# Performance work log

Measured on AMD Instinct MI355X. Metric: run time of the kernel, lower is better.

The kernel has to match this reference:

```python
import jax, jax.numpy as jnp
import numpy as np

B, L, H, D = 4096, 256, 32, 2
LOG_PROB_FACTOR = 0.5

def setup_inputs() -> dict:
    key = jax.random.key(0)
    k0, k1, k2, k3 = jax.random.split(key, 4)
    x = jax.random.randint(k0, (B, L), 0, D)  # spin configs in {0,1}
    Wi = jax.random.normal(k1, (D, 4 * H), dtype=jnp.float32) * 0.1   # input kernel (no bias, flax LSTMCell)
    Wh = jax.random.normal(k2, (H, 4 * H), dtype=jnp.float32) * 0.1   # recurrent kernel
    bh = jnp.zeros((4 * H,), dtype=jnp.float32)                        # recurrent bias
    Wo = jax.random.normal(k3, (H, D), dtype=jnp.float32) * 0.1       # output Dense kernel
    bo = jnp.zeros((D,), dtype=jnp.float32)                            # output Dense bias
    return {"x": x, "Wi": Wi, "Wh": Wh, "bh": bh, "Wo": Wo, "bo": bo}

def reference(x, Wi, Wh, bh, Wo, bo):
    # one-hot of spin t-1 (zeros at t=0); log-prob is read out at spin t.
    x_oh = jax.nn.one_hot(x, D, dtype=Wi.dtype)      # [B, L, D]
    xs = jnp.swapaxes(x_oh, 0, 1)                    # [L, B, D] time-major for scan
    c0 = jnp.zeros((x.shape[0], H), Wi.dtype)
    h0 = jnp.zeros((x.shape[0], H), Wi.dtype)
    inp0 = jnp.zeros((x.shape[0], D), Wi.dtype)      # jnp.zeros(inputDim) initial input

    def step(carry, xt):
        c, h, inp = carry
        gates = inp @ Wi + h @ Wh + bh               # [B, 4H]
        i, f, g, o = jnp.split(gates, 4, axis=-1)    # flax LSTMCell gate order i,f,g,o
        c_new = jax.nn.sigmoid(f) * c + jax.nn.sigmoid(i) * jnp.tanh(g)
        h_new = jax.nn.sigmoid(o) * jnp.tanh(c_new)
        out = jax.nn.elu(h_new @ Wo + bo)            # Dense + actFun, [B, D]
        # log(sum(softmax(out) * onehot)) == gathered log_softmax (stable form)
        logp = jnp.sum(jax.nn.log_softmax(out, axis=-1) * xt, axis=-1)  # [B]
        return (c_new, h_new, xt), logp

    _, logps = jax.lax.scan(step, (c0, h0, inp0), xs)  # logps: [L, B]
    return LOG_PROB_FACTOR * jnp.sum(logps, axis=0)    # [B]
```

## Files before the change

kernel.cpp:

```cpp
#include <hip/hip_runtime.h>


typedef __attribute__((ext_vector_type(8))) short bf16x8;
typedef __attribute__((ext_vector_type(4))) float f32x4;

#define LOG2E 1.4426950408889634f
#define LN2   0.6931471805599453f

__device__ __forceinline__ float fexp2(float x) { return __builtin_amdgcn_exp2f(x); }
__device__ __forceinline__ float flog2(float x) { return __builtin_amdgcn_logf(x); }
__device__ __forceinline__ float frcp(float x)  { return __builtin_amdgcn_rcpf(x); }

__device__ __forceinline__ float fsig(float x)   { return frcp(1.f + fexp2(-LOG2E * x)); }
__device__ __forceinline__ float ftanh_(float x) { return 1.f - 2.f * frcp(fexp2(2.f * LOG2E * x) + 1.f); }
__device__ __forceinline__ float felu(float x)   { return x > 0.f ? x : fexp2(LOG2E * x) - 1.f; }

__device__ __forceinline__ unsigned short f2bf(float f) {
    unsigned u = __builtin_bit_cast(unsigned, f);
    u = (u + 0x7FFFu + ((u >> 16) & 1u)) >> 16;
    return (unsigned short)u;
}

constexpr int Bsz = 4096;

__global__ __launch_bounds__(512, 2) void lstm_mfma8w(
    const int*   __restrict__ x,
    const float* __restrict__ Wi,
    const float* __restrict__ Wh,
    const float* __restrict__ bh,
    const float* __restrict__ Wo,
    const float* __restrict__ bo,
    float*       __restrict__ out)
{
    const int tid  = threadIdx.x;
    const int w    = tid >> 6;
    const int lane = tid & 63;
    const int m    = lane & 15;
    const int oct  = lane >> 4;
    const int rot  = w & 3;
    const int half = w >> 2;
    const int b0   = blockIdx.x * 16;

    __shared__ char   spinT[16][260];
    __shared__ float2 Sbuf[256][16];
    __shared__ short  hbuf[2][16][36];
    __shared__ float  red[8][16];

    {
        const int bl = tid >> 5;
        const int c8 = (tid & 31) * 8;
        const int4* src = reinterpret_cast<const int4*>(x + (b0 + bl) * 256 + c8);
        const int4 v0 = src[0], v1 = src[1];
        const int p0 = (v0.x & 1) | ((v0.y & 1) << 8) | ((v0.z & 1) << 16) | ((v0.w & 1) << 24);
        const int p1 = (v1.x & 1) | ((v1.y & 1) << 8) | ((v1.z & 1) << 16) | ((v1.w & 1) << 24);
        *reinterpret_cast<int*>(&spinT[bl][c8])     = p0;
        *reinterpret_cast<int*>(&spinT[bl][c8 + 4]) = p1;
    }

    bf16x8 wfrag[4];
#pragma unroll
    for (int q = 0; q < 4; ++q) {
        const float gs = (q == 2) ? 2.f * LOG2E : -LOG2E;
        const int colg = 32 * q + 16 * half + ((m + rot) & 15);
#pragma unroll
        for (int j = 0; j < 8; ++j)
            wfrag[q][j] = (short)f2bf(gs * Wh[(oct * 8 + j) * 128 + colg]);
    }
    bf16x8 wofragA;
#pragma unroll
    for (int j = 0; j < 8; ++j)
        wofragA[j] = (m < 2) ? (short)f2bf(Wo[(oct * 8 + j) * 2 + m]) : (short)0;

    const int ucell = 4 * oct + rot + 16 * half;
    float bv0[4], bvd[4];
#pragma unroll
    for (int q = 0; q < 4; ++q) {
        const float gs = (q == 2) ? 2.f * LOG2E : -LOG2E;
        const int colg0 = 32 * q + ucell;
        bv0[q] = gs * (bh[colg0] + Wi[colg0]);
        bvd[q] = gs * (Wi[128 + colg0] - Wi[colg0]);
    }
    const float bo0 = bo[0], bo1 = bo[1];

    float c;
    {
        c = fsig(bh[ucell]) * ftanh_(bh[64 + ucell]);
        const float h0 = fsig(bh[96 + ucell]) * ftanh_(c);
        hbuf[0][m][ucell] = (short)f2bf(h0);
    }
    __syncthreads();

    const f32x4 zero4 = { 0.f, 0.f, 0.f, 0.f };
    f32x4 ccq[4] = { zero4, zero4, zero4, zero4 };
    float spf = (float)spinT[m][0];

    for (int t = 1; t < 256; ++t) {
        const short4* hp =
            reinterpret_cast<const short4*>(&hbuf[(t + 1) & 1][m][8 * oct]);
        const short4 ra = hp[0], rb = hp[1];
        union { bf16x8 v; short4 s[2]; } hu;
        hu.s[0] = ra; hu.s[1] = rb;
        const bf16x8 hfrag = hu.v;

#pragma unroll
        for (int q = 0; q < 4; ++q) ccq[q][0] = fmaf(spf, bvd[q], bv0[q]);

        f32x4 acc[4];
#pragma unroll
        for (int q = 0; q < 4; ++q)
            acc[q] = __builtin_amdgcn_mfma_f32_16x16x32_bf16(wfrag[q], hfrag, ccq[q], 0, 0, 0);

        if (w == 0) {
            const f32x4 hacc =
                __builtin_amdgcn_mfma_f32_16x16x32_bf16(wofragA, hfrag, zero4, 0, 0, 0);
            if (oct == 0) Sbuf[t - 1][m] = make_float2(hacc[0], hacc[1]);
        }

        const float spn = (float)spinT[m][t];

        {
            const float ei = fexp2(acc[0][0]), ef = fexp2(acc[1][0]);
            const float eg = fexp2(acc[2][0]), eo = fexp2(acc[3][0]);
            const float gf = frcp(1.f + ef);
            const float igt = (eg - 1.f) * frcp((1.f + ei) * (1.f + eg));
            c = fmaf(gf, c, igt);
            const float ec = fexp2(2.f * LOG2E * c);
            const float h  = (ec - 1.f) * frcp((1.f + eo) * (1.f + ec));
            hbuf[t & 1][m][ucell] = (short)f2bf(h);
        }

        spf = spn;
        __syncthreads();
    }

    if (w == 0) {
        const short4* hp = reinterpret_cast<const short4*>(&hbuf[1][m][8 * oct]);
        const short4 ra = hp[0], rb = hp[1];
        union { bf16x8 v; short4 s[2]; } hu;
        hu.s[0] = ra; hu.s[1] = rb;
        const f32x4 hacc =
            __builtin_amdgcn_mfma_f32_16x16x32_bf16(wofragA, hu.v, zero4, 0, 0, 0);
        if (oct == 0) Sbuf[255][m] = make_float2(hacc[0], hacc[1]);
    }
    __syncthreads();

    float lp = 0.f;
    {
        const int t0 = (w * 4 + oct) * 8;
#pragma unroll
        for (int i = 0; i < 8; ++i) {
            const int t = t0 + i;
            const float2 sv = Sbuf[t][m];
            const int sp = spinT[m][t];
            const float o0 = felu(sv.x + bo0);
            const float o1 = felu(sv.y + bo1);
            const float mx = fmaxf(o0, o1), mn = fminf(o0, o1);
            const float lse = mx + LN2 * flog2(1.f + fexp2(LOG2E * (mn - mx)));
            lp += (sp ? o1 : o0) - lse;
        }
    }
    lp += __shfl_xor(lp, 16, 64);
    lp += __shfl_xor(lp, 32, 64);
    if (lane < 16) red[w][lane] = lp;
    __syncthreads();
    if (tid < 16) {
        float s = 0.f;
#pragma unroll
        for (int ww = 0; ww < 8; ++ww) s += red[ww][tid];
        out[b0 + tid] = 0.5f * s;
    }
}

extern "C" void kernel_launch(void* const* d_in, const int* in_sizes, int n_in,
                              void* d_out, int out_size, void* d_ws, size_t ws_size,
                              hipStream_t stream) {
    const int*   x  = (const int*)d_in[0];
    const float* Wi = (const float*)d_in[1];
    const float* Wh = (const float*)d_in[2];
    const float* bh = (const float*)d_in[3];
    const float* Wo = (const float*)d_in[4];
    const float* bo = (const float*)d_in[5];
    float* out = (float*)d_out;

    lstm_mfma8w<<<dim3(Bsz / 16), dim3(512), 0, stream>>>(x, Wi, Wh, bh, Wo, bo, out);
}
```

Measured before the change: 146.2 us.

## Split batch into 8-row workgroups of 4 waves with duplicated-h MFMA tiling

Each workgroup now handles 8 batch rows with 256 threads (4 waves) instead of 16 rows with 512 threads, doubling the grid to 512 blocks. The MFMA B operand duplicates the 8 hidden rows into 16 columns, and two accumulator rows per lane hold gates for two cells. The output projection Wo is folded into spare rows of the first gate weight fragment, which removes the separate MFMA. The gate math also shares one reciprocal between the forget and input/tanh terms. The aim is to shorten per-step barrier cost and spread the serial recurrence over more CUs, at the cost of half the MFMA columns being redundant.

After: 153.4 us. +4.9%, slower.

```diff
diff --git a/kernel.cpp b/kernel.cpp
--- a/kernel.cpp
+++ b/kernel.cpp
@@ -23,7 +23,7 @@
 
 constexpr int Bsz = 4096;
 
-__global__ __launch_bounds__(512, 2) void lstm_mfma8w(
+__global__ __launch_bounds__(256, 2) void lstm_mfma2wg(
     const int*   __restrict__ x,
     const float* __restrict__ Wi,
     const float* __restrict__ Wh,
@@ -35,16 +35,16 @@
     const int tid  = threadIdx.x;
     const int w    = tid >> 6;
     const int lane = tid & 63;
-    const int m    = lane & 15;
+    const int n    = lane & 15;
     const int oct  = lane >> 4;
-    const int rot  = w & 3;
-    const int half = w >> 2;
-    const int b0   = blockIdx.x * 16;
+    const int m    = n & 7;
+    const int sel  = n >> 3;
+    const int b0   = blockIdx.x * 8;
 
-    __shared__ char   spinT[16][260];
-    __shared__ float2 Sbuf[256][16];
-    __shared__ short  hbuf[2][16][36];
-    __shared__ float  red[8][16];
+    __shared__ char  spinT[8][260];
+    __shared__ float Sbuf[256 * 8 * 2];
+    __shared__ short hbuf[2][8][40];
+    __shared__ float red[32][8];
 
     {
         const int bl = tid >> 5;
@@ -57,37 +57,38 @@
         *reinterpret_cast<int*>(&spinT[bl][c8 + 4]) = p1;
     }
 
+    const int rho = n & 3;
+    const int oN  = n >> 2;
     bf16x8 wfrag[4];
 #pragma unroll
     for (int q = 0; q < 4; ++q) {
         const float gs = (q == 2) ? 2.f * LOG2E : -LOG2E;
-        const int colg = 32 * q + 16 * half + ((m + rot) & 15);
 #pragma unroll
-        for (int j = 0; j < 8; ++j)
-            wfrag[q][j] = (short)f2bf(gs * Wh[(oct * 8 + j) * 128 + colg]);
+        for (int j = 0; j < 8; ++j) {
+            const int u = 8 * oct + j;
+            float v = 0.f;
+            if (rho < 2)                 v = gs * Wh[u * 128 + 32 * q + 8 * oN + 4 * rho + w];
+            else if (rho == 2 && q == 0 && oN < 2) v = Wo[u * 2 + oN];
+            wfrag[q][j] = (short)f2bf(v);
+        }
     }
-    bf16x8 wofragA;
-#pragma unroll
-    for (int j = 0; j < 8; ++j)
-        wofragA[j] = (m < 2) ? (short)f2bf(Wo[(oct * 8 + j) * 2 + m]) : (short)0;
 
-    const int ucell = 4 * oct + rot + 16 * half;
-    float bv0[4], bvd[4];
+    const int ucell = 8 * oct + 4 * sel + w;
+    float2 bv0[4], bvd[4];
 #pragma unroll
     for (int q = 0; q < 4; ++q) {
         const float gs = (q == 2) ? 2.f * LOG2E : -LOG2E;
-        const int colg0 = 32 * q + ucell;
-        bv0[q] = gs * (bh[colg0] + Wi[colg0]);
-        bvd[q] = gs * (Wi[128 + colg0] - Wi[colg0]);
+        const int c0 = 32 * q + 8 * oct + w;
+        const int c1 = c0 + 4;
+        bv0[q].x = gs * (bh[c0] + Wi[c0]);
+        bvd[q].x = gs * (Wi[128 + c0] - Wi[c0]);
+        bv0[q].y = gs * (bh[c1] + Wi[c1]);
+        bvd[q].y = gs * (Wi[128 + c1] - Wi[c1]);
     }
     const float bo0 = bo[0], bo1 = bo[1];
 
-    float c;
-    {
-        c = fsig(bh[ucell]) * ftanh_(bh[64 + ucell]);
-        const float h0 = fsig(bh[96 + ucell]) * ftanh_(c);
-        hbuf[0][m][ucell] = (short)f2bf(h0);
-    }
+    float c = fsig(bh[ucell]) * ftanh_(bh[64 + ucell]);
+    hbuf[0][m][ucell] = (short)f2bf(fsig(bh[96 + ucell]) * ftanh_(c));
     __syncthreads();
 
     const f32x4 zero4 = { 0.f, 0.f, 0.f, 0.f };
@@ -95,34 +96,38 @@
     float spf = (float)spinT[m][0];
 
     for (int t = 1; t < 256; ++t) {
-        const short4* hp =
-            reinterpret_cast<const short4*>(&hbuf[(t + 1) & 1][m][8 * oct]);
-        const short4 ra = hp[0], rb = hp[1];
-        union { bf16x8 v; short4 s[2]; } hu;
-        hu.s[0] = ra; hu.s[1] = rb;
-        const bf16x8 hfrag = hu.v;
+        const bf16x8 hfrag =
+            *reinterpret_cast<const bf16x8*>(&hbuf[(t + 1) & 1][m][8 * oct]);
 
 #pragma unroll
-        for (int q = 0; q < 4; ++q) ccq[q][0] = fmaf(spf, bvd[q], bv0[q]);
+        for (int q = 0; q < 4; ++q) {
+            ccq[q][0] = fmaf(spf, bvd[q].x, bv0[q].x);
+            ccq[q][1] = fmaf(spf, bvd[q].y, bv0[q].y);
+        }
 
         f32x4 acc[4];
 #pragma unroll
         for (int q = 0; q < 4; ++q)
             acc[q] = __builtin_amdgcn_mfma_f32_16x16x32_bf16(wfrag[q], hfrag, ccq[q], 0, 0, 0);
 
-        if (w == 0) {
-            const f32x4 hacc =
-                __builtin_amdgcn_mfma_f32_16x16x32_bf16(wofragA, hfrag, zero4, 0, 0, 0);
-            if (oct == 0) Sbuf[t - 1][m] = make_float2(hacc[0], hacc[1]);
-        }
+        if (w == 0 && oct < 2 && n < 8)
+            Sbuf[((t - 1) * 8 + m) * 2 + oct] = acc[0][2];
 
         const float spn = (float)spinT[m][t];
 
+        const float g0 = sel ? acc[0][1] : acc[0][0];
+        const float g1 = sel ? acc[1][1] : acc[1][0];
+        const float g2 = sel ? acc[2][1] : acc[2][0];
+        const float g3 = sel ? acc[3][1] : acc[3][0];
+
         {
-            const float ei = fexp2(acc[0][0]), ef = fexp2(acc[1][0]);
-            const float eg = fexp2(acc[2][0]), eo = fexp2(acc[3][0]);
-            const float gf = frcp(1.f + ef);
-            const float igt = (eg - 1.f) * frcp((1.f + ei) * (1.f + eg));
+            const float ei = fexp2(g0), ef = fexp2(g1);
+            const float eg = fexp2(g2), eo = fexp2(g3);
+            const float P = (1.f + ei) * (1.f + eg);
+            const float Q = 1.f + ef;
+            const float R = frcp(P * Q);
+            const float gf  = P * R;
+            const float igt = (eg - 1.f) * Q * R;
             c = fmaf(gf, c, igt);
             const float ec = fexp2(2.f * LOG2E * c);
             const float h  = (ec - 1.f) * frcp((1.f + eo) * (1.f + ec));
@@ -134,39 +139,37 @@
     }
 
     if (w == 0) {
-        const short4* hp = reinterpret_cast<const short4*>(&hbuf[1][m][8 * oct]);
-        const short4 ra = hp[0], rb = hp[1];
-        union { bf16x8 v; short4 s[2]; } hu;
-        hu.s[0] = ra; hu.s[1] = rb;
+        const bf16x8 hfrag = *reinterpret_cast<const bf16x8*>(&hbuf[1][m][8 * oct]);
         const f32x4 hacc =
-            __builtin_amdgcn_mfma_f32_16x16x32_bf16(wofragA, hu.v, zero4, 0, 0, 0);
-        if (oct == 0) Sbuf[255][m] = make_float2(hacc[0], hacc[1]);
+            __builtin_amdgcn_mfma_f32_16x16x32_bf16(wfrag[0], hfrag, zero4, 0, 0, 0);
+        if (oct < 2 && n < 8)
+            Sbuf[(255 * 8 + m) * 2 + oct] = hacc[2];
     }
     __syncthreads();
 
-    float lp = 0.f;
     {
-        const int t0 = (w * 4 + oct) * 8;
+        const int m2 = tid & 7;
+        const int t0 = (tid >> 3) * 8;
+        float lp = 0.f;
 #pragma unroll
         for (int i = 0; i < 8; ++i) {
             const int t = t0 + i;
-            const float2 sv = Sbuf[t][m];
-            const int sp = spinT[m][t];
-            const float o0 = felu(sv.x + bo0);
-            const float o1 = felu(sv.y + bo1);
+            const float S0 = Sbuf[(t * 8 + m2) * 2 + 0] + bo0;
+            const float S1 = Sbuf[(t * 8 + m2) * 2 + 1] + bo1;
+            const int sp = spinT[m2][t];
+            const float o0 = felu(S0);
+            const float o1 = felu(S1);
             const float mx = fmaxf(o0, o1), mn = fminf(o0, o1);
             const float lse = mx + LN2 * flog2(1.f + fexp2(LOG2E * (mn - mx)));
             lp += (sp ? o1 : o0) - lse;
         }
+        red[tid >> 3][m2] = lp;
     }
-    lp += __shfl_xor(lp, 16, 64);
-    lp += __shfl_xor(lp, 32, 64);
-    if (lane < 16) red[w][lane] = lp;
     __syncthreads();
-    if (tid < 16) {
+    if (tid < 8) {
         float s = 0.f;
 #pragma unroll
-        for (int ww = 0; ww < 8; ++ww) s += red[ww][tid];
+        for (int g = 0; g < 32; ++g) s += red[g][tid];
         out[b0 + tid] = 0.5f * s;
     }
 }
@@ -182,5 +185,5 @@
     const float* bo = (const float*)d_in[5];
     float* out = (float*)d_out;
 
-    lstm_mfma8w<<<dim3(Bsz / 16), dim3(512), 0, stream>>>(x, Wi, Wh, bh, Wo, bo, out);
+    lstm_mfma2wg<<<dim3(Bsz / 8), dim3(256), 0, stream>>>(x, Wi, Wh, bh, Wo, bo, out);
 }
```

## Run each LSTM batch pair in a single wavefront with bpermute hidden-state exchange

Applied to the files above, without the earlier changes.

Replaces the 8-wave, 16-sequence block that shared h through LDS with a __syncthreads per step by one 64-lane wavefront handling 2 sequences. The hidden state is swapped between lanes with shfl_xor and ds_bpermute, so the recurrence loop no longer needs a block barrier. Each wave now issues 8 gate MFMAs plus the output MFMA per step for only 2 batch rows, which wastes most of the MFMA N dimension. It also launches 2048 small blocks and relies on many resident waves for throughput. The sigmoid math is reorganised to share one reciprocal across gates.

Result: slower. 169.3 us (+15.8%).

```diff
diff --git a/kernel.cpp b/kernel.cpp
--- a/kernel.cpp
+++ b/kernel.cpp
@@ -23,7 +23,7 @@
 
 constexpr int Bsz = 4096;
 
-__global__ __launch_bounds__(512, 2) void lstm_mfma8w(
+__global__ __launch_bounds__(64, 2) void lstm_bperm(
     const int*   __restrict__ x,
     const float* __restrict__ Wi,
     const float* __restrict__ Wh,
@@ -32,142 +32,157 @@
     const float* __restrict__ bo,
     float*       __restrict__ out)
 {
-    const int tid  = threadIdx.x;
-    const int w    = tid >> 6;
-    const int lane = tid & 63;
-    const int m    = lane & 15;
+    const int lane = threadIdx.x & 63;
+    const int n    = lane & 15;
     const int oct  = lane >> 4;
-    const int rot  = w & 3;
-    const int half = w >> 2;
-    const int b0   = blockIdx.x * 16;
-
-    __shared__ char   spinT[16][260];
-    __shared__ float2 Sbuf[256][16];
-    __shared__ short  hbuf[2][16][36];
-    __shared__ float  red[8][16];
+    const int m    = n & 1;
+    const int r    = (n >> 1) & 3;
+    const int s    = n >> 3;
+    const int b0   = blockIdx.x * 2;
+
+    __shared__ char   spinT[2][260];
+    __shared__ float2 Sbuf[256][2];
 
     {
-        const int bl = tid >> 5;
-        const int c8 = (tid & 31) * 8;
-        const int4* src = reinterpret_cast<const int4*>(x + (b0 + bl) * 256 + c8);
+        const int row = lane >> 5;
+        const int c8  = (lane & 31) * 8;
+        const int4* src = reinterpret_cast<const int4*>(x + (b0 + row) * 256 + c8);
         const int4 v0 = src[0], v1 = src[1];
         const int p0 = (v0.x & 1) | ((v0.y & 1) << 8) | ((v0.z & 1) << 16) | ((v0.w & 1) << 24);
         const int p1 = (v1.x & 1) | ((v1.y & 1) << 8) | ((v1.z & 1) << 16) | ((v1.w & 1) << 24);
-        *reinterpret_cast<int*>(&spinT[bl][c8])     = p0;
-        *reinterpret_cast<int*>(&spinT[bl][c8 + 4]) = p1;
-    }
-
-    bf16x8 wfrag[4];
+        *reinterpret_cast<int*>(&spinT[row][c8])     = p0;
+        *reinterpret_cast<int*>(&spinT[row][c8 + 4]) = p1;
+    }
+
+    bf16x8 wfrag[8];
 #pragma unroll
     for (int q = 0; q < 4; ++q) {
         const float gs = (q == 2) ? 2.f * LOG2E : -LOG2E;
-        const int colg = 32 * q + 16 * half + ((m + rot) & 15);
-#pragma unroll
-        for (int j = 0; j < 8; ++j)
-            wfrag[q][j] = (short)f2bf(gs * Wh[(oct * 8 + j) * 128 + colg]);
-    }
-    bf16x8 wofragA;
+#pragma unroll
+        for (int sx = 0; sx < 2; ++sx)
+#pragma unroll
+            for (int j = 0; j < 8; ++j)
+                wfrag[2 * q + sx][j] =
+                    (short)f2bf(gs * Wh[(8 * oct + j) * 128 + 32 * q + 16 * sx + n]);
+    }
+    bf16x8 wofrag;
 #pragma unroll
     for (int j = 0; j < 8; ++j)
-        wofragA[j] = (m < 2) ? (short)f2bf(Wo[(oct * 8 + j) * 2 + m]) : (short)0;
-
-    const int ucell = 4 * oct + rot + 16 * half;
+        wofrag[j] = (n < 2) ? (short)f2bf(Wo[(8 * oct + j) * 2 + n]) : (short)0;
+
+    const int u = 4 * oct + r + 16 * s;
     float bv0[4], bvd[4];
 #pragma unroll
     for (int q = 0; q < 4; ++q) {
         const float gs = (q == 2) ? 2.f * LOG2E : -LOG2E;
-        const int colg0 = 32 * q + ucell;
-        bv0[q] = gs * (bh[colg0] + Wi[colg0]);
-        bvd[q] = gs * (Wi[128 + colg0] - Wi[colg0]);
+        const int c0 = 32 * q + u;
+        bv0[q] = gs * (bh[c0] + Wi[c0]);
+        bvd[q] = gs * (Wi[128 + c0] - Wi[c0]);
     }
     const float bo0 = bo[0], bo1 = bo[1];
 
-    float c;
-    {
-        c = fsig(bh[ucell]) * ftanh_(bh[64 + ucell]);
-        const float h0 = fsig(bh[96 + ucell]) * ftanh_(c);
-        hbuf[0][m][ucell] = (short)f2bf(h0);
-    }
-    __syncthreads();
+    int badr[4];
+#pragma unroll
+    for (int d = 0; d < 4; ++d)
+        badr[d] = 4 * (m + 4 * (d & 1) + 8 * (oct >> 1) + 16 * (2 * (oct & 1) + (d >> 1)));
+
+    const bool rodd = (r & 1) != 0;
+    const bool rhi  = (r & 2) != 0;
+    const bool shi  = (s != 0);
+
+    auto exchange = [&](float h) -> bf16x8 {
+        const int hv = (int)f2bf(h);
+        const int ot = __shfl_xor(hv, 2, 64);
+        const int lo = rodd ? ot : hv;
+        const int hi = rodd ? hv : ot;
+        const int dw = lo | (hi << 16);
+        union { bf16x8 v; int i[4]; } hf;
+#pragma unroll
+        for (int d = 0; d < 4; ++d)
+            hf.i[d] = __builtin_amdgcn_ds_bpermute(badr[d], dw);
+        return hf.v;
+    };
+
+    auto ex = [&](const f32x4& a, const f32x4& b) -> float {
+        const float a01 = rodd ? a[1] : a[0];
+        const float a23 = rodd ? a[3] : a[2];
+        const float av  = rhi ? a23 : a01;
+        const float b01 = rodd ? b[1] : b[0];
+        const float b23 = rodd ? b[3] : b[2];
+        const float bv  = rhi ? b23 : b01;
+        return shi ? bv : av;
+    };
+
+    float c = fsig(bh[u]) * ftanh_(bh[64 + u]);
+    bf16x8 hfrag = exchange(fsig(bh[96 + u]) * ftanh_(c));
+    float spf = (float)spinT[m][0];
 
     const f32x4 zero4 = { 0.f, 0.f, 0.f, 0.f };
-    f32x4 ccq[4] = { zero4, zero4, zero4, zero4 };
-    float spf = (float)spinT[m][0];
 
     for (int t = 1; t < 256; ++t) {
-        const short4* hp =
-            reinterpret_cast<const short4*>(&hbuf[(t + 1) & 1][m][8 * oct]);
-        const short4 ra = hp[0], rb = hp[1];
-        union { bf16x8 v; short4 s[2]; } hu;
-        hu.s[0] = ra; hu.s[1] = rb;
-        const bf16x8 hfrag = hu.v;
-
-#pragma unroll
-        for (int q = 0; q < 4; ++q) ccq[q][0] = fmaf(spf, bvd[q], bv0[q]);
-
-        f32x4 acc[4];
-#pragma unroll
-        for (int q = 0; q < 4; ++q)
-            acc[q] = __builtin_amdgcn_mfma_f32_16x16x32_bf16(wfrag[q], hfrag, ccq[q], 0, 0, 0);
-
-        if (w == 0) {
-            const f32x4 hacc =
-                __builtin_amdgcn_mfma_f32_16x16x32_bf16(wofragA, hfrag, zero4, 0, 0, 0);
-            if (oct == 0) Sbuf[t - 1][m] = make_float2(hacc[0], hacc[1]);
-        }
-
+        float bias[4];
+#pragma unroll
+        for (int q = 0; q < 4; ++q) bias[q] = fmaf(spf, bvd[q], bv0[q]);
+
+        f32x4 acc[8];
+#pragma unroll
+        for (int tt = 0; tt < 8; ++tt)
+            acc[tt] = __builtin_amdgcn_mfma_f32_16x16x32_bf16(wfrag[tt], hfrag, zero4, 0, 0, 0);
+        const f32x4 hacc =
+            __builtin_amdgcn_mfma_f32_16x16x32_bf16(wofrag, hfrag, zero4, 0, 0, 0);
+
+        if (lane < 2) Sbuf[t - 1][lane] = make_float2(hacc[0], hacc[1]);
         const float spn = (float)spinT[m][t];
 
+        const float g0 = ex(acc[0], acc[1]) + bias[0];
+        const float g1 = ex(acc[2], acc[3]) + bias[1];
+        const float g2 = ex(acc[4], acc[5]) + bias[2];
+        const float g3 = ex(acc[6], acc[7]) + bias[3];
+
+        float h;
         {
-            const float ei = fexp2(acc[0][0]), ef = fexp2(acc[1][0]);
-            const float eg = fexp2(acc[2][0]), eo = fexp2(acc[3][0]);
-            const float gf = frcp(1.f + ef);
-            const float igt = (eg - 1.f) * frcp((1.f + ei) * (1.f + eg));
+            const float ei = fexp2(g0), ef = fexp2(g1);
+            const float eg = fexp2(g2), eo = fexp2(g3);
+            const float P = (1.f + ei) * (1.f + eg);
+            const float Q = 1.f + ef;
+            const float R = frcp(P * Q);
+            const float gf  = P * R;
+            const float igt = (eg - 1.f) * Q * R;
             c = fmaf(gf, c, igt);
             const float ec = fexp2(2.f * LOG2E * c);
-            const float h  = (ec - 1.f) * frcp((1.f + eo) * (1.f + ec));
-            hbuf[t & 1][m][ucell] = (short)f2bf(h);
+            h = (ec - 1.f) * frcp((1.f + eo) * (1.f + ec));
         }
-
+        hfrag = exchange(h);
         spf = spn;
-        __syncthreads();
-    }
-
-    if (w == 0) {
-        const short4* hp = reinterpret_cast<const short4*>(&hbuf[1][m][8 * oct]);
-        const short4 ra = hp[0], rb = hp[1];
-        union { bf16x8 v; short4 s[2]; } hu;
-        hu.s[0] = ra; hu.s[1] = rb;
+    }
+
+    {
         const f32x4 hacc =
-            __builtin_amdgcn_mfma_f32_16x16x32_bf16(wofragA, hu.v, zero4, 0, 0, 0);
-        if (oct == 0) Sbuf[255][m] = make_float2(hacc[0], hacc[1]);
-    }
-    __syncthreads();
-
-    float lp = 0.f;
+            __builtin_amdgcn_mfma_f32_16x16x32_bf16(wofrag, hfrag, zero4, 0, 0, 0);
+        if (lane < 2) Sbuf[255][lane] = make_float2(hacc[0], hacc[1]);
+    }
+
     {
-        const int t0 = (w * 4 + oct) * 8;
+        const int m2 = lane & 1;
+        const int t0 = (lane >> 1) * 8;
+        float lp = 0.f;
 #pragma unroll
         for (int i = 0; i < 8; ++i) {
             const int t = t0 + i;
-            const float2 sv = Sbuf[t][m];
-            const int sp = spinT[m][t];
+            const float2 sv = Sbuf[t][m2];
+            const int sp = spinT[m2][t];
             const float o0 = felu(sv.x + bo0);
             const float o1 = felu(sv.y + bo1);
             const float mx = fmaxf(o0, o1), mn = fminf(o0, o1);
             const float lse = mx + LN2 * flog2(1.f + fexp2(LOG2E * (mn - mx)));
             lp += (sp ? o1 : o0) - lse;
         }
-    }
-    lp += __shfl_xor(lp, 16, 64);
-    lp += __shfl_xor(lp, 32, 64);
-    if (lane < 16) red[w][lane] = lp;
-    __syncthreads();
-    if (tid < 16) {
-        float s = 0.f;
-#pragma unroll
-        for (int ww = 0; ww < 8; ++ww) s += red[ww][tid];
-        out[b0 + tid] = 0.5f * s;
+        lp += __shfl_xor(lp, 2, 64);
+        lp += __shfl_xor(lp, 4, 64);
+        lp += __shfl_xor(lp, 8, 64);
+        lp += __shfl_xor(lp, 16, 64);
+        lp += __shfl_xor(lp, 32, 64);
+        if (lane < 2) out[b0 + lane] = 0.5f * lp;
     }
 }
 
@@ -182,5 +197,5 @@
     const float* bo = (const float*)d_in[5];
     float* out = (float*)d_out;
 
-    lstm_mfma8w<<<dim3(Bsz / 16), dim3(512), 0, stream>>>(x, Wi, Wh, bh, Wo, bo, out);
+    lstm_bperm<<<dim3(Bsz / 2), dim3(64), 0, stream>>>(x, Wi, Wh, bh, Wo, bo, out);
 }
```

## Unroll LSTM time loop by two, rotate output MFMA across waves, merge reciprocals

Applied to the files above, without the earlier changes.

The recurrence loop is unrolled two steps at a time with compile-time double-buffer indices. Spins are loaded two per LDS read, and the h fragment is read with a single 16-byte load after padding rows to 40 shorts. The per-step output projection MFMA now rotates across the 8 waves instead of always running on wave 0, which evens out the critical path before each barrier. The forget-gate and input-gate reciprocals are combined into one rcp at the cost of a few extra multiplies, which may slightly change rounding or overflow behaviour.

After: 136.9 us. 1.07x faster.

```diff
diff --git a/kernel.cpp b/kernel.cpp
--- a/kernel.cpp
+++ b/kernel.cpp
@@ -23,7 +23,7 @@
 
 constexpr int Bsz = 4096;
 
-__global__ __launch_bounds__(512, 2) void lstm_mfma8w(
+__global__ __launch_bounds__(512, 2) void lstm_r10(
     const int*   __restrict__ x,
     const float* __restrict__ Wi,
     const float* __restrict__ Wh,
@@ -43,7 +43,7 @@
 
     __shared__ char   spinT[16][260];
     __shared__ float2 Sbuf[256][16];
-    __shared__ short  hbuf[2][16][36];
+    __shared__ short  hbuf[2][16][40];
     __shared__ float  red[8][16];
 
     {
@@ -76,31 +76,22 @@
 #pragma unroll
     for (int q = 0; q < 4; ++q) {
         const float gs = (q == 2) ? 2.f * LOG2E : -LOG2E;
-        const int colg0 = 32 * q + ucell;
-        bv0[q] = gs * (bh[colg0] + Wi[colg0]);
-        bvd[q] = gs * (Wi[128 + colg0] - Wi[colg0]);
+        const int c0 = 32 * q + ucell;
+        bv0[q] = gs * (bh[c0] + Wi[c0]);
+        bvd[q] = gs * (Wi[128 + c0] - Wi[c0]);
     }
     const float bo0 = bo[0], bo1 = bo[1];
 
-    float c;
-    {
-        c = fsig(bh[ucell]) * ftanh_(bh[64 + ucell]);
-        const float h0 = fsig(bh[96 + ucell]) * ftanh_(c);
-        hbuf[0][m][ucell] = (short)f2bf(h0);
-    }
+    float c = fsig(bh[ucell]) * ftanh_(bh[64 + ucell]);
+    hbuf[0][m][ucell] = (short)f2bf(fsig(bh[96 + ucell]) * ftanh_(c));
     __syncthreads();
 
     const f32x4 zero4 = { 0.f, 0.f, 0.f, 0.f };
     f32x4 ccq[4] = { zero4, zero4, zero4, zero4 };
-    float spf = (float)spinT[m][0];
 
-    for (int t = 1; t < 256; ++t) {
-        const short4* hp =
-            reinterpret_cast<const short4*>(&hbuf[(t + 1) & 1][m][8 * oct]);
-        const short4 ra = hp[0], rb = hp[1];
-        union { bf16x8 v; short4 s[2]; } hu;
-        hu.s[0] = ra; hu.s[1] = rb;
-        const bf16x8 hfrag = hu.v;
+    auto step = [&](const int t, const int rb, const int wb, const float spf) {
+        const bf16x8 hfrag =
+            *reinterpret_cast<const bf16x8*>(&hbuf[rb][m][8 * oct]);
 
 #pragma unroll
         for (int q = 0; q < 4; ++q) ccq[q][0] = fmaf(spf, bvd[q], bv0[q]);
@@ -110,36 +101,42 @@
         for (int q = 0; q < 4; ++q)
             acc[q] = __builtin_amdgcn_mfma_f32_16x16x32_bf16(wfrag[q], hfrag, ccq[q], 0, 0, 0);
 
-        if (w == 0) {
+        if (((t - 1) & 7) == w) {
             const f32x4 hacc =
                 __builtin_amdgcn_mfma_f32_16x16x32_bf16(wofragA, hfrag, zero4, 0, 0, 0);
             if (oct == 0) Sbuf[t - 1][m] = make_float2(hacc[0], hacc[1]);
         }
 
-        const float spn = (float)spinT[m][t];
-
         {
             const float ei = fexp2(acc[0][0]), ef = fexp2(acc[1][0]);
             const float eg = fexp2(acc[2][0]), eo = fexp2(acc[3][0]);
-            const float gf = frcp(1.f + ef);
-            const float igt = (eg - 1.f) * frcp((1.f + ei) * (1.f + eg));
+            const float P = (1.f + ei) * (1.f + eg);
+            const float Q = 1.f + ef;
+            const float R = frcp(P * Q);
+            const float gf  = P * R;
+            const float igt = (eg - 1.f) * Q * R;
             c = fmaf(gf, c, igt);
             const float ec = fexp2(2.f * LOG2E * c);
             const float h  = (ec - 1.f) * frcp((1.f + eo) * (1.f + ec));
-            hbuf[t & 1][m][ucell] = (short)f2bf(h);
+            hbuf[wb][m][ucell] = (short)f2bf(h);
         }
+        __syncthreads();
+    };
 
-        spf = spn;
-        __syncthreads();
+    unsigned sp2 = *reinterpret_cast<const unsigned short*>(&spinT[m][0]);
+    for (int tb = 1; tb < 255; tb += 2) {
+        const unsigned sp2n =
+            *reinterpret_cast<const unsigned short*>(&spinT[m][tb + 1]);
+        step(tb,     0, 1, (float)(sp2 & 0xFFu));
+        step(tb + 1, 1, 0, (float)(sp2 >> 8));
+        sp2 = sp2n;
     }
+    step(255, 0, 1, (float)(sp2 & 0xFFu));
 
-    if (w == 0) {
-        const short4* hp = reinterpret_cast<const short4*>(&hbuf[1][m][8 * oct]);
-        const short4 ra = hp[0], rb = hp[1];
-        union { bf16x8 v; short4 s[2]; } hu;
-        hu.s[0] = ra; hu.s[1] = rb;
+    if (w == 7) {
+        const bf16x8 hfrag = *reinterpret_cast<const bf16x8*>(&hbuf[1][m][8 * oct]);
         const f32x4 hacc =
-            __builtin_amdgcn_mfma_f32_16x16x32_bf16(wofragA, hu.v, zero4, 0, 0, 0);
+            __builtin_amdgcn_mfma_f32_16x16x32_bf16(wofragA, hfrag, zero4, 0, 0, 0);
         if (oct == 0) Sbuf[255][m] = make_float2(hacc[0], hacc[1]);
     }
     __syncthreads();
@@ -182,5 +179,5 @@
     const float* bo = (const float*)d_in[5];
     float* out = (float*)d_out;
 
-    lstm_mfma8w<<<dim3(Bsz / 16), dim3(512), 0, stream>>>(x, Wi, Wh, bh, Wo, bo, out);
+    lstm_r10<<<dim3(Bsz / 16), dim3(512), 0, stream>>>(x, Wi, Wh, bh, Wo, bo, out);
 }
```
